# Kernel optimization log

Hardware: AMD Instinct MI355X
Metric: run time of the kernel (lower is better)

The kernel has to match this reference:

```python
import jax, jax.numpy as jnp
import numpy as np

B, S, M, D, H, DH = 2, 1024, 1024, 1024, 16, 64
K = S + M                 # key length
R = 2 * K - 1             # relative position table width
EPS = 1e-5


def layer_norm(x, gamma, beta):
    mu = jnp.mean(x, axis=-1, keepdims=True)
    var = jnp.mean(jnp.square(x - mu), axis=-1, keepdims=True)
    return (x - mu) * jax.lax.rsqrt(var + EPS) * gamma + beta


def skew(q_pos, mem_len):
    # q_pos: (B, H, L, R) with R = 2*k_len - 1
    b, h, L, r = q_pos.shape
    pad = jnp.full((b, h, L, 1), -jnp.inf, q_pos.dtype)
    x = jnp.concatenate([q_pos, pad], axis=-1).reshape(b, h, L * (r + 1))
    x = x[..., : L * r].reshape(b, h, L, r)
    k_len = (r + 1) // 2
    start = k_len - 1 - mem_len
    return x[..., start : start + k_len]  # (B, H, L, k_len)


def setup_inputs() -> dict:
    key = jax.random.key(0)
    ks = jax.random.split(key, 9)
    hidden = jax.random.normal(ks[0], (B, S, D), jnp.float32)
    memory = jax.random.normal(ks[1], (B, M, D), jnp.float32)
    pos_emb = jax.random.normal(ks[2], (B, R, DH), jnp.float32)
    # causal mask: query i may attend keys j <= i + M ; True = blocked
    mask = jnp.arange(K)[None, :] > (jnp.arange(S)[:, None] + M)
    sc = 1.0 / np.sqrt(D)
    Wq = jax.random.normal(ks[3], (D, H * DH), jnp.float32) * sc
    Wk = jax.random.normal(ks[4], (D, H * DH), jnp.float32) * sc
    Wv = jax.random.normal(ks[5], (D, H * DH), jnp.float32) * sc
    Wo = jax.random.normal(ks[6], (H * DH, D), jnp.float32) * sc
    gamma = jnp.ones((D,), jnp.float32)
    beta = jnp.zeros((D,), jnp.float32)
    return {"hidden": hidden, "pos_emb": pos_emb, "memory": memory,
            "mask": mask, "Wq": Wq, "Wk": Wk, "Wv": Wv, "Wo": Wo,
            "gamma": gamma, "beta": beta}


def reference(hidden, pos_emb, memory, mask, Wq, Wk, Wv, Wo, gamma, beta):
    mem_len = memory.shape[1]
    combined = jnp.concatenate([memory, hidden], axis=1)  # (B, K, D)
    h_ln = layer_norm(hidden, gamma, beta)                # pre-LN
    c_ln = layer_norm(combined, gamma, beta)
    q = (h_ln @ Wq).reshape(B, S, H, DH).transpose(0, 2, 1, 3)  # (B,H,S,DH)
    k = (c_ln @ Wk).reshape(B, K, H, DH).transpose(0, 2, 1, 3)  # (B,H,K,DH)
    v = (c_ln @ Wv).reshape(B, K, H, DH).transpose(0, 2, 1, 3)
    score = jnp.einsum('bhsd,bhkd->bhsk', q, k)                  # (B,H,S,K)
    q_pos = jnp.einsum('bhsd,brd->bhsr', q, pos_emb)             # (B,H,S,R)
    score = (score + skew(q_pos, mem_len)) * (1.0 / np.sqrt(D))
    score = jnp.where(mask[None, None], -jnp.inf, score)
    p = jax.nn.softmax(score, axis=-1)
    attn = jnp.einsum('bhsk,bhkd->bshd', p, v).reshape(B, S, H * DH)
    out = attn @ Wo
    return h_ln + out
```

## Files before the change

### kernel.cpp

```cpp
#include <hip/hip_runtime.h>
#include <hip/hip_bf16.h>

#define B_ 2
#define S_ 1024
#define M_ 1024
#define D_ 1024
#define H_ 16
#define DH_ 64
#define K_ 2048
#define R_ 4095

#define NEG_BIG (-1e30f)

typedef unsigned short u16;
typedef short short8 __attribute__((ext_vector_type(8)));
typedef float f32x4 __attribute__((ext_vector_type(4)));

__device__ __forceinline__ u16 f2bf(float f) {
  __hip_bfloat16 h = __float2bfloat16(f);
  return *reinterpret_cast<u16*>(&h);
}
__device__ __forceinline__ float bf2f(u16 u) {
  __hip_bfloat16 h;
  *reinterpret_cast<u16*>(&h) = u;
  return __bfloat162float(h);
}

__device__ __forceinline__ void gll16(const void* g, const void* l) {
  __builtin_amdgcn_global_load_lds(
      (const __attribute__((address_space(1))) unsigned int*)g,
      (__attribute__((address_space(3))) unsigned int*)l, 16, 0, 0);
}

__device__ __forceinline__ f32x4 mfma16(short8 a, short8 b, f32x4 c) {
  return __builtin_amdgcn_mfma_f32_16x16x32_bf16(a, b, c, 0, 0, 0);
}

__global__ __launch_bounds__(256) void prep_kernel(
    const float* __restrict__ hidden, const float* __restrict__ memory,
    const float* __restrict__ gamma, const float* __restrict__ beta,
    u16* __restrict__ cln,
    const float* __restrict__ W0, const float* __restrict__ W1,
    const float* __restrict__ W2, const float* __restrict__ W3,
    u16* __restrict__ O0, u16* __restrict__ O1,
    u16* __restrict__ O2, u16* __restrict__ O3,
    const float* __restrict__ pos, u16* __restrict__ posb) {
  __shared__ u16 tile[64][66];
  __shared__ float red[8];
  const int bx = blockIdx.x;
  const int t = threadIdx.x;

  if (bx < 4096) {
    const int b = bx >> 11;
    const int idx = bx & (K_ - 1);
    const float* src = (idx < M_)
        ? memory + (size_t)(b * M_ + idx) * D_
        : hidden + (size_t)(b * S_ + (idx - M_)) * D_;
    const int lane = t & 63, w = t >> 6;
    float4 rv = ((const float4*)src)[t];
    float s = rv.x + rv.y + rv.z + rv.w;
    float ss = rv.x * rv.x + rv.y * rv.y + rv.z * rv.z + rv.w * rv.w;
#pragma unroll
    for (int m = 1; m < 64; m <<= 1) {
      s += __shfl_xor(s, m, 64);
      ss += __shfl_xor(ss, m, 64);
    }
    if (lane == 0) { red[w] = s; red[4 + w] = ss; }
    __syncthreads();
    s = red[0] + red[1] + red[2] + red[3];
    ss = red[4] + red[5] + red[6] + red[7];
    const float mu = s * (1.0f / D_);
    const float var = ss * (1.0f / D_) - mu * mu;
    const float rstd = rsqrtf(var + 1e-5f);
    float4 gv = ((const float4*)gamma)[t];
    float4 bv = ((const float4*)beta)[t];
    ushort4 ov;
    ov.x = f2bf((rv.x - mu) * rstd * gv.x + bv.x);
    ov.y = f2bf((rv.y - mu) * rstd * gv.y + bv.y);
    ov.z = f2bf((rv.z - mu) * rstd * gv.z + bv.z);
    ov.w = f2bf((rv.w - mu) * rstd * gv.w + bv.w);
    ((ushort4*)(cln + (size_t)bx * D_))[t] = ov;
    return;
  }
  if (bx < 5120) {
    const int z = (bx - 4096) >> 8;
    const int rem = (bx - 4096) & 255;
    const float* in; u16* out;
    switch (z) {
      case 0:  in = W0; out = O0; break;
      case 1:  in = W1; out = O1; break;
      case 2:  in = W2; out = O2; break;
      default: in = W3; out = O3; break;
    }
    const int tx = t & 63, ty = t >> 6;
    const int k0 = (rem & 15) * 64, n0 = (rem >> 4) * 64;
#pragma unroll
    for (int i = ty; i < 64; i += 4)
      tile[i][tx] = f2bf(in[(size_t)(k0 + i) * D_ + n0 + tx]);
    __syncthreads();
#pragma unroll
    for (int i = ty; i < 64; i += 4)
      out[(size_t)(n0 + i) * D_ + k0 + tx] = tile[tx][i];
    return;
  }
  const int i = (bx - 5120) * 256 + t;
  const int n4 = B_ * R_ * 64 / 4;
  if (i < n4) {
    float4 v = ((const float4*)pos)[i];
    ushort4 o;
    o.x = f2bf(v.x); o.y = f2bf(v.y); o.z = f2bf(v.z); o.w = f2bf(v.w);
    ((ushort4*)posb)[i] = o;
  }
}

__device__ __forceinline__ int maprow_hidden(int r) {
  return r + ((r >> 10) << 10) + M_;
}

__global__ __launch_bounds__(256, 2) void gemm_qkv_kernel(
    const u16* __restrict__ A, const u16* __restrict__ Bt,
    u16* __restrict__ qb, u16* __restrict__ kb, u16* __restrict__ vbT) {
  __shared__ __align__(16) u16 As[128 * 32];
  __shared__ __align__(16) u16 Bs[128 * 32];
  const int t = threadIdx.x;
  const int lane = t & 63, w = t >> 6;
  const int wm = w >> 1, wn = w & 1;
  const int qd = lane >> 4, lr = lane & 15;
  const int m0 = blockIdx.y * 128, n0 = blockIdx.x * 128;

  if (n0 < 1024 && !(m0 & 1024)) return;

  const u16* Ag0 = A + (size_t)(m0 + (t >> 2)) * 1024 + (t & 3) * 8;
  const u16* Ag1 = Ag0 + (size_t)64 * 1024;
  const u16* Bg0 = Bt + (size_t)(n0 + (t >> 2)) * 1024 + (t & 3) * 8;
  const u16* Bg1 = Bg0 + (size_t)64 * 1024;

  f32x4 acc[4][4];
#pragma unroll
  for (int mt = 0; mt < 4; mt++)
#pragma unroll
    for (int nt = 0; nt < 4; nt++) acc[mt][nt] = (f32x4){0.f, 0.f, 0.f, 0.f};

  for (int kt = 0; kt < 1024; kt += 32) {
    gll16(Ag0 + kt, As + w * 512);
    gll16(Ag1 + kt, As + 2048 + w * 512);
    gll16(Bg0 + kt, Bs + w * 512);
    gll16(Bg1 + kt, Bs + 2048 + w * 512);
    __syncthreads();
    short8 af[4], bfr[4];
#pragma unroll
    for (int mt = 0; mt < 4; mt++)
      af[mt] = *(const short8*)&As[(wm * 64 + mt * 16 + lr) * 32 + qd * 8];
#pragma unroll
    for (int nt = 0; nt < 4; nt++)
      bfr[nt] = *(const short8*)&Bs[(wn * 64 + nt * 16 + lr) * 32 + qd * 8];
#pragma unroll
    for (int mt = 0; mt < 4; mt++)
#pragma unroll
      for (int nt = 0; nt < 4; nt++)
        acc[mt][nt] = mfma16(af[mt], bfr[nt], acc[mt][nt]);
    __syncthreads();
  }

#pragma unroll
  for (int mt = 0; mt < 4; mt++)
#pragma unroll
    for (int nt = 0; nt < 4; nt++) {
      const int colb = n0 + wn * 64 + nt * 16;
      const int rowb = m0 + wm * 64 + mt * 16 + qd * 4;
      if (colb < 1024) {
        const int qrow = ((rowb >> 11) << 10) | (rowb & 1023);
#pragma unroll
        for (int r = 0; r < 4; r++)
          qb[(size_t)(qrow + r) * 1024 + colb + lr] = f2bf(acc[mt][nt][r] * 0.03125f);
      } else if (colb < 2048) {
        const int key = rowb & (K_ - 1);
        const int bq = rowb >> 11;
#pragma unroll
        for (int r = 0; r < 4; r++)
          kb[(size_t)(bq * K_ + key + r) * 1024 + (colb - 1024) + lr] = f2bf(acc[mt][nt][r]);
      } else {
        const int nn = colb - 2048 + lr;
        const int bh = ((rowb >> 11) << 4) | (nn >> 6);
        const int dh = nn & 63;
        const int key = rowb & (K_ - 1);
        ushort4 pk;
        pk.x = f2bf(acc[mt][nt][0]);
        pk.y = f2bf(acc[mt][nt][1]);
        pk.z = f2bf(acc[mt][nt][2]);
        pk.w = f2bf(acc[mt][nt][3]);
        *(ushort4*)&vbT[((size_t)bh * 64 + dh) * K_ + key] = pk;
      }
    }
}

__global__ __launch_bounds__(256, 2) void out_gemm_kernel(
    const u16* __restrict__ A, const u16* __restrict__ Bt,
    const u16* __restrict__ resid, float* __restrict__ Cf) {
  __shared__ __align__(16) u16 As[128 * 32];
  __shared__ __align__(16) u16 Bs[64 * 32];
  const int t = threadIdx.x;
  const int lane = t & 63, w = t >> 6;
  const int wm = w >> 1, wn = w & 1;
  const int qd = lane >> 4, lr = lane & 15;
  const int m0 = blockIdx.y * 128, n0 = blockIdx.x * 64;

  const u16* Ag0 = A + (size_t)(m0 + (t >> 2)) * 1024 + (t & 3) * 8;
  const u16* Ag1 = Ag0 + (size_t)64 * 1024;
  const u16* Bg0 = Bt + (size_t)(n0 + (t >> 2)) * 1024 + (t & 3) * 8;

  f32x4 acc[4][2];
#pragma unroll
  for (int mt = 0; mt < 4; mt++)
#pragma unroll
    for (int nt = 0; nt < 2; nt++) acc[mt][nt] = (f32x4){0.f, 0.f, 0.f, 0.f};

  for (int kt = 0; kt < 1024; kt += 32) {
    gll16(Ag0 + kt, As + w * 512);
    gll16(Ag1 + kt, As + 2048 + w * 512);
    gll16(Bg0 + kt, Bs + w * 512);
    __syncthreads();
    short8 af[4], bfr[2];
#pragma unroll
    for (int mt = 0; mt < 4; mt++)
      af[mt] = *(const short8*)&As[(wm * 64 + mt * 16 + lr) * 32 + qd * 8];
#pragma unroll
    for (int nt = 0; nt < 2; nt++)
      bfr[nt] = *(const short8*)&Bs[(wn * 32 + nt * 16 + lr) * 32 + qd * 8];
#pragma unroll
    for (int mt = 0; mt < 4; mt++)
#pragma unroll
      for (int nt = 0; nt < 2; nt++)
        acc[mt][nt] = mfma16(af[mt], bfr[nt], acc[mt][nt]);
    __syncthreads();
  }

#pragma unroll
  for (int mt = 0; mt < 4; mt++)
#pragma unroll
    for (int nt = 0; nt < 2; nt++)
#pragma unroll
      for (int r = 0; r < 4; r++) {
        const int row = m0 + wm * 64 + mt * 16 + qd * 4 + r;
        const int col = n0 + wn * 32 + nt * 16 + lr;
        float v = acc[mt][nt][r] + bf2f(resid[(size_t)maprow_hidden(row) * 1024 + col]);
        Cf[(size_t)row * 1024 + col] = v;
      }
}

__global__ __launch_bounds__(256, 2) void attn_kernel(
    const u16* __restrict__ qb, const u16* __restrict__ kb,
    const u16* __restrict__ vbT, const u16* __restrict__ pos,
    u16* __restrict__ ab) {
  __shared__ __align__(16) u16 Ks[2][64 * 64];
  __shared__ __align__(16) u16 Vt[2][64 * 64];
  __shared__ __align__(16) u16 Ps[192 * 64];
  __shared__ __align__(16) u16 Pt[4][16 * 68];

  const int t = threadIdx.x;
  const int lane = t & 63, w = t >> 6;
  const int qd = lane >> 4, lr = lane & 15;
  const int h = blockIdx.y;
  const int b = blockIdx.z;
  int qt = blockIdx.x;
  if (b) qt = 15 - qt;
  const int i0 = qt * 64;

  const int swz = ((t & 7) ^ ((t >> 3) & 7)) * 8;
  const int c0 = (qd ^ (lr & 7)) * 8;
  const int c1 = c0 ^ 32;
  const int base0 = 960 - i0;
  const int row8 = t >> 3;

#pragma unroll
  for (int rd = 0; rd < 2; rd++)
    gll16(qb + (size_t)(b * S_ + i0 + rd * 32 + row8) * 1024 + h * 64 + swz,
          &Ks[1][0] + rd * 2048 + w * 512);
#pragma unroll
  for (int rd = 0; rd < 2; rd++) {
    gll16(kb + (size_t)(b * K_ + rd * 32 + row8) * 1024 + h * 64 + swz,
          &Ks[0][0] + rd * 2048 + w * 512);
    gll16(vbT + (size_t)((b * H_ + h) * 64 + rd * 32 + row8) * K_ + swz,
          &Vt[0][0] + rd * 2048 + w * 512);
  }
#pragma unroll
  for (int rd = 0; rd < 4; rd++)
    gll16(pos + (size_t)(b * R_ + base0 + rd * 32 + row8) * 64 + swz,
          Ps + rd * 2048 + w * 512);
  __syncthreads();
  const short8 aQ0 = *(const short8*)&Ks[1][(w * 16 + lr) * 64 + c0];
  const short8 aQ1 = *(const short8*)&Ks[1][(w * 16 + lr) * 64 + c1];

  f32x4 accO[4];
#pragma unroll
  for (int d = 0; d < 4; d++) accO[d] = (f32x4){0.f, 0.f, 0.f, 0.f};
  float lsum[4];
#pragma unroll
  for (int r = 0; r < 4; r++) lsum[r] = 0.f;

  const int bw0 = 48 - w * 16;
  const int jmax = min(K_, i0 + 64 + M_);
  int sa = 0, sb = 1, sc = 2;
  int cur = 0;

  for (int j0 = 0, tt = 0; j0 < jmax; j0 += 64, tt++) {
    __syncthreads();
    if (j0 + 64 < jmax) {
      const int nxt = cur ^ 1;
#pragma unroll
      for (int rd = 0; rd < 2; rd++) {
        gll16(kb + (size_t)(b * K_ + j0 + 64 + rd * 32 + row8) * 1024 + h * 64 + swz,
              &Ks[nxt][0] + rd * 2048 + w * 512);
        gll16(vbT + (size_t)((b * H_ + h) * 64 + rd * 32 + row8) * K_ + j0 + 64 + swz,
              &Vt[nxt][0] + rd * 2048 + w * 512);
      }
    }
#pragma unroll
    for (int rd = 0; rd < 2; rd++)
      gll16(pos + (size_t)(b * R_ + base0 + 64 * tt + 128 + rd * 32 + row8) * 64 + swz,
            Ps + (sc * 64 + rd * 32) * 64 + w * 512);

    f32x4 sqk[4];
#pragma unroll
    for (int kc = 0; kc < 4; kc++) {
      const short8 bK0 = *(const short8*)&Ks[cur][(kc * 16 + lr) * 64 + c0];
      const short8 bK1 = *(const short8*)&Ks[cur][(kc * 16 + lr) * 64 + c1];
      f32x4 z = {0.f, 0.f, 0.f, 0.f};
      z = mfma16(aQ0, bK0, z);
      sqk[kc] = mfma16(aQ1, bK1, z);
    }
    f32x4 zp[5];
#pragma unroll
    for (int pc = 0; pc < 5; pc++) {
      const int xb = bw0 + pc * 16;
      const int slab = (xb >= 64) ? sb : sa;
      const int pb = slab * 64 + (xb & 63);
      const short8 bP0 = *(const short8*)&Ps[(pb + lr) * 64 + c0];
      const short8 bP1 = *(const short8*)&Ps[(pb + lr) * 64 + c1];
      f32x4 z = {0.f, 0.f, 0.f, 0.f};
      z = mfma16(aQ0, bP0, z);
      zp[pc] = mfma16(aQ1, bP1, z);
    }

    const bool tail = (j0 + 63 > i0 + w * 16 + M_);
    float p[4][4];
#pragma unroll
    for (int r = 0; r < 4; r++) {
      const int iL = qd * 4 + r;
      const int d = 15 + lr - iL;
      const int srcl = qd * 16 + (d & 15);
      const bool hi = (d >> 4) & 1;
      float g0 = __shfl(zp[0][r], srcl, 64);
      float g1 = __shfl(zp[1][r], srcl, 64);
      float g2 = __shfl(zp[2][r], srcl, 64);
      float g3 = __shfl(zp[3][r], srcl, 64);
      float g4 = __shfl(zp[4][r], srcl, 64);
      float s0 = sqk[0][r] + (hi ? g1 : g0);
      float s1 = sqk[1][r] + (hi ? g2 : g1);
      float s2 = sqk[2][r] + (hi ? g3 : g2);
      float s3 = sqk[3][r] + (hi ? g4 : g3);
      if (tail) {
        const int key = j0 + lr, lim = i0 + w * 16 + iL + M_;
        if (key      > lim) s0 = NEG_BIG;
        if (key + 16 > lim) s1 = NEG_BIG;
        if (key + 32 > lim) s2 = NEG_BIG;
        if (key + 48 > lim) s3 = NEG_BIG;
      }
      p[0][r] = __expf(s0);
      p[1][r] = __expf(s1);
      p[2][r] = __expf(s2);
      p[3][r] = __expf(s3);
      lsum[r] += p[0][r] + p[1][r] + p[2][r] + p[3][r];
    }

#pragma unroll
    for (int r = 0; r < 4; r++) {
      const int base = (qd * 4 + r) * 68 + lr;
      Pt[w][base +  0] = f2bf(p[0][r]);
      Pt[w][base + 16] = f2bf(p[1][r]);
      Pt[w][base + 32] = f2bf(p[2][r]);
      Pt[w][base + 48] = f2bf(p[3][r]);
    }
    __asm__ volatile("s_waitcnt lgkmcnt(0)" ::: "memory");
    const short8 aP0 = *(const short8*)&Pt[w][lr * 68 + qd * 8];
    const short8 aP1 = *(const short8*)&Pt[w][lr * 68 + 32 + qd * 8];

#pragma unroll
    for (int d2 = 0; d2 < 4; d2++) {
      const short8 bV0 = *(const short8*)&Vt[cur][(d2 * 16 + lr) * 64 + c0];
      const short8 bV1 = *(const short8*)&Vt[cur][(d2 * 16 + lr) * 64 + c1];
      accO[d2] = mfma16(aP0, bV0, accO[d2]);
      accO[d2] = mfma16(aP1, bV1, accO[d2]);
    }

    const int so = sa; sa = sb; sb = sc; sc = so;
    cur ^= 1;
  }

  float inv[4];
#pragma unroll
  for (int r = 0; r < 4; r++) {
#pragma unroll
    for (int msk = 1; msk < 16; msk <<= 1) lsum[r] += __shfl_xor(lsum[r], msk, 64);
    inv[r] = 1.0f / lsum[r];
  }
#pragma unroll
  for (int d2 = 0; d2 < 4; d2++)
#pragma unroll
    for (int r = 0; r < 4; r++) {
      const int iG = i0 + w * 16 + qd * 4 + r;
      ab[(size_t)(b * S_ + iG) * 1024 + h * 64 + d2 * 16 + lr] = f2bf(accO[d2][r] * inv[r]);
    }
}

extern "C" void kernel_launch(void* const* d_in, const int* in_sizes, int n_in,
                              void* d_out, int out_size, void* d_ws, size_t ws_size,
                              hipStream_t stream) {
  const float* hidden = (const float*)d_in[0];
  const float* pos    = (const float*)d_in[1];
  const float* memory = (const float*)d_in[2];
  const float* Wq = (const float*)d_in[4];
  const float* Wk = (const float*)d_in[5];
  const float* Wv = (const float*)d_in[6];
  const float* Wo = (const float*)d_in[7];
  const float* gamma = (const float*)d_in[8];
  const float* beta  = (const float*)d_in[9];

  char* ws = (char*)d_ws;
  u16* cln  = (u16*)(ws);
  u16* qb   = (u16*)(ws + 8388608);
  u16* kb   = (u16*)(ws + 12582912);
  u16* vbT  = (u16*)(ws + 20971520);
  u16* ab   = (u16*)(ws + 29360128);
  u16* WqT  = (u16*)(ws + 33554432);
  u16* WkT  = WqT + 1048576;
  u16* WvT  = WkT + 1048576;
  u16* WoT  = WvT + 1048576;
  u16* posb = (u16*)(ws + 41943040);

  prep_kernel<<<dim3(5632), 256, 0, stream>>>(
      hidden, memory, gamma, beta, cln,
      Wq, Wk, Wv, Wo, WqT, WkT, WvT, WoT, pos, posb);
  gemm_qkv_kernel<<<dim3(24, 32), 256, 0, stream>>>(cln, WqT, qb, kb, vbT);
  attn_kernel<<<dim3(S_ / 64, H_, B_), 256, 0, stream>>>(qb, kb, vbT, posb, ab);
  out_gemm_kernel<<<dim3(16, 16), 256, 0, stream>>>(ab, WoT, cln, (float*)d_out);
}
```

Before: 212.6 us.

## Split attention over key halves with merge kernel; widen QKV GEMM K-tile

The attention kernel now splits each query tile's key range into a memory half and a hidden half. This doubles the block count, and a new merge kernel sums the unnormalized partial outputs and row sums. Positional-embedding fragments are read straight from global memory into registers instead of through a rotating LDS slab, and the occupancy hint rises to 3 blocks per CU. The QKV GEMM moves to a 64-wide K tile with swizzled LDS to halve the number of barriers. The split adds an extra kernel launch, partial-output traffic, and a bf16 rounding of the partial sums. It also reuses the weight workspace region for the partial buffers.

```diff
diff --git a/kernel.cpp b/kernel.cpp
--- a/kernel.cpp
+++ b/kernel.cpp
@@ -120,20 +120,19 @@
 __global__ __launch_bounds__(256, 2) void gemm_qkv_kernel(
     const u16* __restrict__ A, const u16* __restrict__ Bt,
     u16* __restrict__ qb, u16* __restrict__ kb, u16* __restrict__ vbT) {
-  __shared__ __align__(16) u16 As[128 * 32];
-  __shared__ __align__(16) u16 Bs[128 * 32];
+  __shared__ __align__(16) u16 As[128 * 64];
+  __shared__ __align__(16) u16 Bs[128 * 64];
   const int t = threadIdx.x;
   const int lane = t & 63, w = t >> 6;
   const int wm = w >> 1, wn = w & 1;
   const int qd = lane >> 4, lr = lane & 15;
   const int m0 = blockIdx.y * 128, n0 = blockIdx.x * 128;
-
   if (n0 < 1024 && !(m0 & 1024)) return;
 
-  const u16* Ag0 = A + (size_t)(m0 + (t >> 2)) * 1024 + (t & 3) * 8;
-  const u16* Ag1 = Ag0 + (size_t)64 * 1024;
-  const u16* Bg0 = Bt + (size_t)(n0 + (t >> 2)) * 1024 + (t & 3) * 8;
-  const u16* Bg1 = Bg0 + (size_t)64 * 1024;
+  const int swz = ((t & 7) ^ ((t >> 3) & 7)) * 8;
+  const int c0 = (qd ^ (lr & 7)) * 8;
+  const int c1 = c0 ^ 32;
+  const int row8 = (t >> 3) & 7;
 
   f32x4 acc[4][4];
 #pragma unroll
@@ -141,24 +140,32 @@
 #pragma unroll
     for (int nt = 0; nt < 4; nt++) acc[mt][nt] = (f32x4){0.f, 0.f, 0.f, 0.f};
 
-  for (int kt = 0; kt < 1024; kt += 32) {
-    gll16(Ag0 + kt, As + w * 512);
-    gll16(Ag1 + kt, As + 2048 + w * 512);
-    gll16(Bg0 + kt, Bs + w * 512);
-    gll16(Bg1 + kt, Bs + 2048 + w * 512);
-    __syncthreads();
-    short8 af[4], bfr[4];
+  for (int kt = 0; kt < 1024; kt += 64) {
+#pragma unroll
+    for (int p = 0; p < 4; p++) {
+      const int ra = w * 32 + p * 8 + row8;
+      gll16(A + (size_t)(m0 + ra) * 1024 + kt + swz, As + (w * 32 + p * 8) * 64);
+      gll16(Bt + (size_t)(n0 + ra) * 1024 + kt + swz, Bs + (w * 32 + p * 8) * 64);
+    }
+    __syncthreads();
+    short8 a0[4], a1[4], b0[4], b1[4];
+#pragma unroll
+    for (int mt = 0; mt < 4; mt++) {
+      a0[mt] = *(const short8*)&As[(wm * 64 + mt * 16 + lr) * 64 + c0];
+      a1[mt] = *(const short8*)&As[(wm * 64 + mt * 16 + lr) * 64 + c1];
+    }
+#pragma unroll
+    for (int nt = 0; nt < 4; nt++) {
+      b0[nt] = *(const short8*)&Bs[(wn * 64 + nt * 16 + lr) * 64 + c0];
+      b1[nt] = *(const short8*)&Bs[(wn * 64 + nt * 16 + lr) * 64 + c1];
+    }
 #pragma unroll
     for (int mt = 0; mt < 4; mt++)
-      af[mt] = *(const short8*)&As[(wm * 64 + mt * 16 + lr) * 32 + qd * 8];
-#pragma unroll
-    for (int nt = 0; nt < 4; nt++)
-      bfr[nt] = *(const short8*)&Bs[(wn * 64 + nt * 16 + lr) * 32 + qd * 8];
-#pragma unroll
-    for (int mt = 0; mt < 4; mt++)
-#pragma unroll
-      for (int nt = 0; nt < 4; nt++)
-        acc[mt][nt] = mfma16(af[mt], bfr[nt], acc[mt][nt]);
+#pragma unroll
+      for (int nt = 0; nt < 4; nt++) {
+        acc[mt][nt] = mfma16(a0[mt], b0[nt], acc[mt][nt]);
+        acc[mt][nt] = mfma16(a1[mt], b1[nt], acc[mt][nt]);
+      }
     __syncthreads();
   }
 
@@ -248,45 +255,41 @@
       }
 }
 
-__global__ __launch_bounds__(256, 2) void attn_kernel(
+__global__ __launch_bounds__(256, 3) void attn_kernel(
     const u16* __restrict__ qb, const u16* __restrict__ kb,
-    const u16* __restrict__ vbT, const u16* __restrict__ pos,
-    u16* __restrict__ ab) {
+    const u16* __restrict__ vbT, const u16* __restrict__ posb,
+    u16* __restrict__ abp, float* __restrict__ lp) {
   __shared__ __align__(16) u16 Ks[2][64 * 64];
   __shared__ __align__(16) u16 Vt[2][64 * 64];
-  __shared__ __align__(16) u16 Ps[192 * 64];
   __shared__ __align__(16) u16 Pt[4][16 * 68];
 
   const int t = threadIdx.x;
   const int lane = t & 63, w = t >> 6;
   const int qd = lane >> 4, lr = lane & 15;
-  const int h = blockIdx.y;
-  const int b = blockIdx.z;
-  int qt = blockIdx.x;
-  if (b) qt = 15 - qt;
+
+  int s, qt, h, b;
+  const int e = blockIdx.x;
+  if (e < 512) { s = 0; qt = e & 15; h = (e >> 4) & 15; b = e >> 8; }
+  else { const int e2 = e - 512; s = 1; qt = 15 - (e2 >> 5); h = e2 & 15; b = (e2 >> 4) & 1; }
   const int i0 = qt * 64;
+  const int k0 = s << 10;
+  const int k1 = s ? min(K_, i0 + 64 + M_) : 1024;
 
   const int swz = ((t & 7) ^ ((t >> 3) & 7)) * 8;
   const int c0 = (qd ^ (lr & 7)) * 8;
   const int c1 = c0 ^ 32;
-  const int base0 = 960 - i0;
   const int row8 = t >> 3;
-
-#pragma unroll
-  for (int rd = 0; rd < 2; rd++)
+  const int bw0 = 48 - w * 16;
+
+#pragma unroll
+  for (int rd = 0; rd < 2; rd++) {
     gll16(qb + (size_t)(b * S_ + i0 + rd * 32 + row8) * 1024 + h * 64 + swz,
           &Ks[1][0] + rd * 2048 + w * 512);
-#pragma unroll
-  for (int rd = 0; rd < 2; rd++) {
-    gll16(kb + (size_t)(b * K_ + rd * 32 + row8) * 1024 + h * 64 + swz,
+    gll16(kb + (size_t)(b * K_ + k0 + rd * 32 + row8) * 1024 + h * 64 + swz,
           &Ks[0][0] + rd * 2048 + w * 512);
-    gll16(vbT + (size_t)((b * H_ + h) * 64 + rd * 32 + row8) * K_ + swz,
+    gll16(vbT + (size_t)((b * H_ + h) * 64 + rd * 32 + row8) * K_ + k0 + swz,
           &Vt[0][0] + rd * 2048 + w * 512);
   }
-#pragma unroll
-  for (int rd = 0; rd < 4; rd++)
-    gll16(pos + (size_t)(b * R_ + base0 + rd * 32 + row8) * 64 + swz,
-          Ps + rd * 2048 + w * 512);
   __syncthreads();
   const short8 aQ0 = *(const short8*)&Ks[1][(w * 16 + lr) * 64 + c0];
   const short8 aQ1 = *(const short8*)&Ks[1][(w * 16 + lr) * 64 + c1];
@@ -298,14 +301,19 @@
 #pragma unroll
   for (int r = 0; r < 4; r++) lsum[r] = 0.f;
 
-  const int bw0 = 48 - w * 16;
-  const int jmax = min(K_, i0 + 64 + M_);
-  int sa = 0, sb = 1, sc = 2;
   int cur = 0;
-
-  for (int j0 = 0, tt = 0; j0 < jmax; j0 += 64, tt++) {
-    __syncthreads();
-    if (j0 + 64 < jmax) {
+  for (int j0 = k0; j0 < k1; j0 += 64) {
+    short8 bP0[5], bP1[5];
+#pragma unroll
+    for (int pc = 0; pc < 5; pc++) {
+      const int prow = 960 - i0 + j0 + bw0 + pc * 16 + lr;
+      const u16* pp = posb + ((size_t)b * R_ + prow) * 64 + qd * 8;
+      bP0[pc] = *(const short8*)pp;
+      bP1[pc] = *(const short8*)(pp + 32);
+    }
+    __syncthreads();
+
+    if (j0 + 64 < k1) {
       const int nxt = cur ^ 1;
 #pragma unroll
       for (int rd = 0; rd < 2; rd++) {
@@ -315,10 +323,6 @@
               &Vt[nxt][0] + rd * 2048 + w * 512);
       }
     }
-#pragma unroll
-    for (int rd = 0; rd < 2; rd++)
-      gll16(pos + (size_t)(b * R_ + base0 + 64 * tt + 128 + rd * 32 + row8) * 64 + swz,
-            Ps + (sc * 64 + rd * 32) * 64 + w * 512);
 
     f32x4 sqk[4];
 #pragma unroll
@@ -332,14 +336,9 @@
     f32x4 zp[5];
 #pragma unroll
     for (int pc = 0; pc < 5; pc++) {
-      const int xb = bw0 + pc * 16;
-      const int slab = (xb >= 64) ? sb : sa;
-      const int pb = slab * 64 + (xb & 63);
-      const short8 bP0 = *(const short8*)&Ps[(pb + lr) * 64 + c0];
-      const short8 bP1 = *(const short8*)&Ps[(pb + lr) * 64 + c1];
       f32x4 z = {0.f, 0.f, 0.f, 0.f};
-      z = mfma16(aQ0, bP0, z);
-      zp[pc] = mfma16(aQ1, bP1, z);
+      z = mfma16(aQ0, bP0[pc], z);
+      zp[pc] = mfma16(aQ1, bP1[pc], z);
     }
 
     const bool tail = (j0 + 63 > i0 + w * 16 + M_);
@@ -392,25 +391,45 @@
       accO[d2] = mfma16(aP0, bV0, accO[d2]);
       accO[d2] = mfma16(aP1, bV1, accO[d2]);
     }
-
-    const int so = sa; sa = sb; sb = sc; sc = so;
     cur ^= 1;
   }
 
-  float inv[4];
 #pragma unroll
   for (int r = 0; r < 4; r++) {
 #pragma unroll
     for (int msk = 1; msk < 16; msk <<= 1) lsum[r] += __shfl_xor(lsum[r], msk, 64);
-    inv[r] = 1.0f / lsum[r];
+    const int iG = i0 + w * 16 + qd * 4 + r;
+    if (lr == 0) lp[(((s << 1) + b) * 16 + h) * 1024 + iG] = lsum[r];
   }
 #pragma unroll
   for (int d2 = 0; d2 < 4; d2++)
 #pragma unroll
     for (int r = 0; r < 4; r++) {
       const int iG = i0 + w * 16 + qd * 4 + r;
-      ab[(size_t)(b * S_ + iG) * 1024 + h * 64 + d2 * 16 + lr] = f2bf(accO[d2][r] * inv[r]);
-    }
+      abp[(size_t)(((s << 1) + b) * S_ + iG) * 1024 + h * 64 + d2 * 16 + lr] =
+          f2bf(accO[d2][r]);
+    }
+}
+
+__global__ __launch_bounds__(256) void merge_kernel(
+    const u16* __restrict__ abp, const float* __restrict__ lp,
+    u16* __restrict__ ab) {
+  const int rowg = blockIdx.x;
+  const int b = rowg >> 10, row = rowg & 1023;
+  const int t = threadIdx.x;
+  const int c = t * 4;
+  const int h = t >> 4;
+  const float l0 = lp[(b * 16 + h) * 1024 + row];
+  const float l1 = lp[((2 + b) * 16 + h) * 1024 + row];
+  const float inv = 1.0f / (l0 + l1);
+  ushort4 a0 = *(const ushort4*)&abp[((size_t)(b * S_ + row)) * 1024 + c];
+  ushort4 a1 = *(const ushort4*)&abp[((size_t)((2 + b) * S_ + row)) * 1024 + c];
+  ushort4 o;
+  o.x = f2bf((bf2f(a0.x) + bf2f(a1.x)) * inv);
+  o.y = f2bf((bf2f(a0.y) + bf2f(a1.y)) * inv);
+  o.z = f2bf((bf2f(a0.z) + bf2f(a1.z)) * inv);
+  o.w = f2bf((bf2f(a0.w) + bf2f(a1.w)) * inv);
+  *(ushort4*)&ab[((size_t)(b * S_ + row)) * 1024 + c] = o;
 }
 
 extern "C" void kernel_launch(void* const* d_in, const int* in_sizes, int n_in,
@@ -432,16 +451,19 @@
   u16* kb   = (u16*)(ws + 12582912);
   u16* vbT  = (u16*)(ws + 20971520);
   u16* ab   = (u16*)(ws + 29360128);
-  u16* WqT  = (u16*)(ws + 33554432);
+  u16* WoT  = (u16*)(ws + 33554432);
+  u16* WqT  = (u16*)(ws + 35651584);
   u16* WkT  = WqT + 1048576;
   u16* WvT  = WkT + 1048576;
-  u16* WoT  = WvT + 1048576;
-  u16* posb = (u16*)(ws + 41943040);
+  u16* abp  = (u16*)(ws + 35651584);
+  float* lp = (float*)(ws + 45088768);
+  u16* posb = (u16*)(ws + 44040192);
 
   prep_kernel<<<dim3(5632), 256, 0, stream>>>(
       hidden, memory, gamma, beta, cln,
       Wq, Wk, Wv, Wo, WqT, WkT, WvT, WoT, pos, posb);
   gemm_qkv_kernel<<<dim3(24, 32), 256, 0, stream>>>(cln, WqT, qb, kb, vbT);
-  attn_kernel<<<dim3(S_ / 64, H_, B_), 256, 0, stream>>>(qb, kb, vbT, posb, ab);
+  attn_kernel<<<dim3(1024), 256, 0, stream>>>(qb, kb, vbT, posb, abp, lp);
+  merge_kernel<<<dim3(B_ * S_), 256, 0, stream>>>(abp, lp, ab);
   out_gemm_kernel<<<dim3(16, 16), 256, 0, stream>>>(ab, WoT, cln, (float*)d_out);
 }
```

After: 229.0 us. +7.7%, slower.
